# Optimization experiments

Hardware: AMD Instinct MI355X
Metric: run time of the kernel (lower is better)

Reference implementation:

```python
import jax, jax.numpy as jnp
import numpy as np

TAU = 2.0          # LIF membrane time constant
V_THRESHOLD = 1.0  # spikingjelly LIFNode default
V_RESET = 0.0      # hard reset target (spikingjelly default)
ATAN_ALPHA = 2.0   # surrogate.ATan default alpha

T, B, L, D_IN, D_OUT = 16, 32, 128, 512, 512


@jax.custom_vjp
def atan_spike(x):
    # Heaviside forward; ATan surrogate gradient in backward.
    return (x >= 0.0).astype(x.dtype)

def _atan_spike_fwd(x):
    return atan_spike(x), x

def _atan_spike_bwd(x, g):
    # d/dx [ (1/pi) * atan(pi/2 * alpha * x) + 1/2 ]
    grad = (ATAN_ALPHA / 2.0) / (1.0 + (jnp.pi / 2.0 * ATAN_ALPHA * x) ** 2)
    return (g * grad,)

atan_spike.defvjp(_atan_spike_fwd, _atan_spike_bwd)


def lif_multistep(h):
    """Multi-step LIF over leading time axis. h: [T, B, L, H] -> spikes [T, B, L, H].
    spikingjelly LIFNode (decay_input=True, hard reset, detach_reset=True):
      v = v + (x - (v - v_reset)) / tau
      s = heaviside(v - v_threshold)   (ATan surrogate grad)
      v = v_reset * s_detached + v * (1 - s_detached)
    """
    def step(v, x_t):
        v = v + (x_t - (v - V_RESET)) / TAU
        s = atan_spike(v - V_THRESHOLD)
        s_d = jax.lax.stop_gradient(s)  # detach_reset=True
        v = V_RESET * s_d + v * (1.0 - s_d)
        return v, s

    v0 = jnp.zeros_like(h[0])
    _, spikes = jax.lax.scan(step, v0, h)
    return spikes


def setup_inputs() -> dict:
    key = jax.random.key(0)
    kx, kw, kb = jax.random.split(key, 3)
    x = jax.random.normal(kx, (T, B, L, D_IN), dtype=jnp.float32)
    # nn.Linear init: U(-1/sqrt(fan_in), 1/sqrt(fan_in))
    bound = 1.0 / np.sqrt(D_IN)
    W = jax.random.uniform(kw, (D_OUT, D_IN), minval=-bound, maxval=bound, dtype=jnp.float32)
    b = jax.random.uniform(kb, (D_OUT,), minval=-bound, maxval=bound, dtype=jnp.float32)
    return {"x": x, "W": W, "b": b}


def reference(x, W, b):
    # Linear over flattened (T*B) dims == per-element projection, then LIF.
    h = jnp.einsum("tbld,hd->tblh", x, W) + b  # [T, B, L, D_OUT]
    return lif_multistep(h)
```

## Files before the change

### kernel.cpp

```cpp
#include <hip/hip_runtime.h>

using f32x4 = __attribute__((ext_vector_type(4))) float;
using s16x8 = __attribute__((ext_vector_type(8))) short;

constexpr int T_STEPS = 16;
constexpr int BLTOT   = 4096;
constexpr int KDIM    = 512;
constexpr int NDIM    = 512;

constexpr int BM = 128, BN = 128, BK = 32;
constexpr int ROWB  = 80;
constexpr int COMP  = 128 * ROWB;
constexpr int BBASE = 3 * COMP;


__device__ __forceinline__ void split3_write(char* lds, float4 v, int off) {
  unsigned u[4], u1[4], u2[4];
  float r1[4], r2[4];
#pragma unroll
  for (int e = 0; e < 4; ++e) {
    float ve = ((const float*)&v)[e];
    u[e]  = __float_as_uint(ve);
    r1[e] = ve - __uint_as_float(u[e] & 0xFFFF0000u);
    u1[e] = __float_as_uint(r1[e]);
    r2[e] = r1[e] - __uint_as_float(u1[e] & 0xFFFF0000u);
    u2[e] = __float_as_uint(r2[e]);
  }
  uint2 hp, mp, lp;
  hp.x = (u[0]  >> 16) | (u[1]  & 0xFFFF0000u);
  hp.y = (u[2]  >> 16) | (u[3]  & 0xFFFF0000u);
  mp.x = (u1[0] >> 16) | (u1[1] & 0xFFFF0000u);
  mp.y = (u1[2] >> 16) | (u1[3] & 0xFFFF0000u);
  lp.x = (u2[0] >> 16) | (u2[1] & 0xFFFF0000u);
  lp.y = (u2[2] >> 16) | (u2[3] & 0xFFFF0000u);
  *(uint2*)(lds + off)            = hp;
  *(uint2*)(lds + off + COMP)     = mp;
  *(uint2*)(lds + off + 2 * COMP) = lp;
}

__global__ __launch_bounds__(256, 2)
void fused_mfma_lif(const float* __restrict__ x, const float* __restrict__ W,
                    const float* __restrict__ bias, float* __restrict__ out) {
  __shared__ __align__(16) char lds[6 * COMP];

  const int tid  = threadIdx.x;
  const int lane = tid & 63;
  const int wv   = tid >> 6;
  const int wm   = wv >> 1;
  const int wn   = wv & 1;
  const int bl0  = blockIdx.x * 8;
  const int n0   = blockIdx.y * BN;

  const float* aptr[4];
  const float* bptr[4];
  int aw[4], bw[4];
#pragma unroll
  for (int i = 0; i < 4; ++i) {
    int f  = i * 256 + tid;
    int r  = f >> 3;
    int kq = (f & 7) * 4;
    int t  = ((r >> 4) & 3) * 4 + (r & 3);
    int bl = (r >> 6) * 4 + ((r >> 2) & 3);
    aptr[i] = x + (size_t)(t * BLTOT + bl0 + bl) * KDIM + kq;
    bptr[i] = W + (size_t)(n0 + r) * KDIM + kq;
    aw[i] = r * ROWB + kq * 2;
    bw[i] = BBASE + r * ROWB + kq * 2;
  }

  f32x4 acc[4][4];
#pragma unroll
  for (int a = 0; a < 4; ++a)
#pragma unroll
    for (int b = 0; b < 4; ++b) acc[a][b] = (f32x4)(0.0f);

  const int arow = (wm * 64 + (lane & 15)) * ROWB + (lane >> 4) * 16;
  const int brow = BBASE + (wn * 64 + (lane & 15)) * ROWB + (lane >> 4) * 16;

  float4 ar[4], br[4];
#pragma unroll
  for (int i = 0; i < 4; ++i) {
    ar[i] = *(const float4*)(aptr[i]);
    br[i] = *(const float4*)(bptr[i]);
  }

  for (int it = 0; it < 16; ++it) {
    __syncthreads();
#pragma unroll
    for (int i = 0; i < 4; ++i) {
      split3_write(lds, ar[i], aw[i]);
      split3_write(lds, br[i], bw[i]);
    }
    __syncthreads();

    if (it < 15) {
      const int ko = (it + 1) * BK;
#pragma unroll
      for (int i = 0; i < 4; ++i) {
        ar[i] = *(const float4*)(aptr[i] + ko);
        br[i] = *(const float4*)(bptr[i] + ko);
      }
    }

    s16x8 bf[4][3];
#pragma unroll
    for (int nf = 0; nf < 4; ++nf)
#pragma unroll
      for (int c = 0; c < 3; ++c)
        bf[nf][c] = *(const s16x8*)(lds + brow + nf * 16 * ROWB + c * COMP);

#pragma unroll
    for (int mf = 0; mf < 4; ++mf) {
      s16x8 af[3];
#pragma unroll
      for (int c = 0; c < 3; ++c)
        af[c] = *(const s16x8*)(lds + arow + mf * 16 * ROWB + c * COMP);
#pragma unroll
      for (int nf = 0; nf < 4; ++nf) {
        f32x4 c0 = acc[mf][nf];
        c0 = __builtin_amdgcn_mfma_f32_16x16x32_bf16(af[2], bf[nf][0], c0, 0, 0, 0);
        c0 = __builtin_amdgcn_mfma_f32_16x16x32_bf16(af[0], bf[nf][2], c0, 0, 0, 0);
        c0 = __builtin_amdgcn_mfma_f32_16x16x32_bf16(af[1], bf[nf][1], c0, 0, 0, 0);
        c0 = __builtin_amdgcn_mfma_f32_16x16x32_bf16(af[1], bf[nf][0], c0, 0, 0, 0);
        c0 = __builtin_amdgcn_mfma_f32_16x16x32_bf16(af[0], bf[nf][1], c0, 0, 0, 0);
        c0 = __builtin_amdgcn_mfma_f32_16x16x32_bf16(af[0], bf[nf][0], c0, 0, 0, 0);
        acc[mf][nf] = c0;
      }
    }
  }

  const int G   = lane >> 4;
  const int bl  = bl0 + wm * 4 + G;
  const int col = lane & 15;
#pragma unroll
  for (int nf = 0; nf < 4; ++nf) {
    const int n = n0 + wn * 64 + nf * 16 + col;
    const float bb = bias[n];
    float v = 0.0f;
#pragma unroll
    for (int t = 0; t < T_STEPS; ++t) {
      const float h = ((const float*)&acc[t >> 2][nf])[t & 3] + bb;
      float vn = v + (h - v) * 0.5f;
      const bool s = (vn >= 1.0f);
      out[(size_t)(t * BLTOT + bl) * NDIM + n] = s ? 1.0f : 0.0f;
      v = s ? 0.0f : vn;
    }
  }
}

extern "C" void kernel_launch(void* const* d_in, const int* in_sizes, int n_in,
                              void* d_out, int out_size, void* d_ws, size_t ws_size,
                              hipStream_t stream) {
  const float* x = (const float*)d_in[0];
  const float* W = (const float*)d_in[1];
  const float* b = (const float*)d_in[2];
  float* out = (float*)d_out;

  dim3 grid(BLTOT / 8, NDIM / BN);
  fused_mfma_lif<<<grid, 256, 0, stream>>>(x, W, b, out);
}
```

Measured before the change: 448.4 us.

## Pre-split operands into bf16x3 fragment layout in workspace, load directly to LDS

Adds two pre-pass kernels that split x and W into high, mid and low bf16 parts and store them in an MFMA-fragment-ready layout in the workspace. The GEMM+LIF kernel then streams these fragments straight into LDS with global_load_lds, and uses a swizzled block order to improve L2 reuse across the four N-blocks. This removes the repeated per-block split arithmetic and the register-to-LDS scatter from the main loop. In exchange it writes and re-reads a roughly 200 MB workspace, and the main loop is single-buffered with two barriers per iteration. The old fused kernel is kept as a fallback when the workspace is too small.

New measurement: 415.1 us. -7.4%, faster.

```diff
diff --git a/kernel.cpp b/kernel.cpp
--- a/kernel.cpp
+++ b/kernel.cpp
@@ -8,64 +8,91 @@
 constexpr int KDIM    = 512;
 constexpr int NDIM    = 512;
 
-constexpr int BM = 128, BN = 128, BK = 32;
-constexpr int ROWB  = 80;
-constexpr int COMP  = 128 * ROWB;
-constexpr int BBASE = 3 * COMP;
-
-
-__device__ __forceinline__ void split3_write(char* lds, float4 v, int off) {
-  unsigned u[4], u1[4], u2[4];
-  float r1[4], r2[4];
-#pragma unroll
-  for (int e = 0; e < 4; ++e) {
-    float ve = ((const float*)&v)[e];
-    u[e]  = __float_as_uint(ve);
-    r1[e] = ve - __uint_as_float(u[e] & 0xFFFF0000u);
-    u1[e] = __float_as_uint(r1[e]);
-    r2[e] = r1[e] - __uint_as_float(u1[e] & 0xFFFF0000u);
-    u2[e] = __float_as_uint(r2[e]);
-  }
-  uint2 hp, mp, lp;
-  hp.x = (u[0]  >> 16) | (u[1]  & 0xFFFF0000u);
-  hp.y = (u[2]  >> 16) | (u[3]  & 0xFFFF0000u);
-  mp.x = (u1[0] >> 16) | (u1[1] & 0xFFFF0000u);
-  mp.y = (u1[2] >> 16) | (u1[3] & 0xFFFF0000u);
-  lp.x = (u2[0] >> 16) | (u2[1] & 0xFFFF0000u);
-  lp.y = (u2[2] >> 16) | (u2[3] & 0xFFFF0000u);
-  *(uint2*)(lds + off)            = hp;
-  *(uint2*)(lds + off + COMP)     = mp;
-  *(uint2*)(lds + off + 2 * COMP) = lp;
+constexpr size_t B_BYTES = 32ull * 16 * 3 * 1024;
+constexpr size_t A_BYTES = 512ull * 8 * 16 * 3 * 1024;
+constexpr size_t ABASE   = B_BYTES;
+constexpr size_t WS_NEED = A_BYTES + B_BYTES;
+
+
+__device__ __forceinline__ void split8(const float* e, uint4& hp, uint4& mp, uint4& lp) {
+  unsigned h[8], m[8], l[8];
+#pragma unroll
+  for (int j = 0; j < 8; ++j) {
+    const float f = e[j];
+    const unsigned u = __float_as_uint(f);
+    h[j] = u >> 16;
+    const float r1 = f - __uint_as_float(u & 0xFFFF0000u);
+    const unsigned u1 = __float_as_uint(r1);
+    m[j] = u1 >> 16;
+    const float r2 = r1 - __uint_as_float(u1 & 0xFFFF0000u);
+    l[j] = __float_as_uint(r2) >> 16;
+  }
+  hp = make_uint4(h[0] | (h[1] << 16), h[2] | (h[3] << 16),
+                  h[4] | (h[5] << 16), h[6] | (h[7] << 16));
+  mp = make_uint4(m[0] | (m[1] << 16), m[2] | (m[3] << 16),
+                  m[4] | (m[5] << 16), m[6] | (m[7] << 16));
+  lp = make_uint4(l[0] | (l[1] << 16), l[2] | (l[3] << 16),
+                  l[4] | (l[5] << 16), l[6] | (l[7] << 16));
+}
+
+__global__ void split_w(const float* __restrict__ W, char* __restrict__ ws) {
+  const int tid = threadIdx.x;
+  const int wid = blockIdx.x * 4 + (tid >> 6);
+  const int lane = tid & 63;
+  const int nt = wid >> 4, ks = wid & 15;
+  const int q = lane & 15, g = lane >> 4;
+  const float* src = W + (size_t)(nt * 16 + q) * KDIM + ks * 32 + g * 8;
+  float e[8];
+  *(float4*)&e[0] = *(const float4*)src;
+  *(float4*)&e[4] = *(const float4*)(src + 4);
+  uint4 hp, mp, lp;
+  split8(e, hp, mp, lp);
+  char* dst = ws + (size_t)wid * 3072 + lane * 16;
+  *(uint4*)(dst)        = hp;
+  *(uint4*)(dst + 1024) = mp;
+  *(uint4*)(dst + 2048) = lp;
+}
+
+__global__ void split_x(const float* __restrict__ x, char* __restrict__ ws) {
+  const int tid = threadIdx.x;
+  const int wid = blockIdx.x * 4 + (tid >> 6);
+  const int lane = tid & 63;
+  const int ks = wid & 15, mtile = wid >> 4;
+  const int mt = mtile & 7, mb = mtile >> 3;
+  const int q = lane & 15, g = lane >> 4;
+  const int t  = (mt & 3) * 4 + (q & 3);
+  const int bl = mb * 8 + (mt >> 2) * 4 + (q >> 2);
+  const float* src = x + (size_t)(t * BLTOT + bl) * KDIM + ks * 32 + g * 8;
+  float e[8];
+  *(float4*)&e[0] = *(const float4*)src;
+  *(float4*)&e[4] = *(const float4*)(src + 4);
+  uint4 hp, mp, lp;
+  split8(e, hp, mp, lp);
+  char* dst = ws + ABASE + (size_t)wid * 3072 + lane * 16;
+  *(uint4*)(dst)        = hp;
+  *(uint4*)(dst + 1024) = mp;
+  *(uint4*)(dst + 2048) = lp;
 }
 
 __global__ __launch_bounds__(256, 2)
-void fused_mfma_lif(const float* __restrict__ x, const float* __restrict__ W,
-                    const float* __restrict__ bias, float* __restrict__ out) {
-  __shared__ __align__(16) char lds[6 * COMP];
+void gemm_lif_frag(const char* __restrict__ wsB, const char* __restrict__ wsA,
+                   const float* __restrict__ bias, float* __restrict__ out) {
+  __shared__ __align__(16) char lds[48 * 1024];
 
   const int tid  = threadIdx.x;
   const int lane = tid & 63;
   const int wv   = tid >> 6;
-  const int wm   = wv >> 1;
-  const int wn   = wv & 1;
-  const int bl0  = blockIdx.x * 8;
-  const int n0   = blockIdx.y * BN;
-
-  const float* aptr[4];
-  const float* bptr[4];
-  int aw[4], bw[4];
-#pragma unroll
-  for (int i = 0; i < 4; ++i) {
-    int f  = i * 256 + tid;
-    int r  = f >> 3;
-    int kq = (f & 7) * 4;
-    int t  = ((r >> 4) & 3) * 4 + (r & 3);
-    int bl = (r >> 6) * 4 + ((r >> 2) & 3);
-    aptr[i] = x + (size_t)(t * BLTOT + bl0 + bl) * KDIM + kq;
-    bptr[i] = W + (size_t)(n0 + r) * KDIM + kq;
-    aw[i] = r * ROWB + kq * 2;
-    bw[i] = BBASE + r * ROWB + kq * 2;
-  }
+  const int wm   = wv >> 1, wn = wv & 1;
+
+  const int w    = blockIdx.x;
+  const int orig = (w & 7) * 256 + (w >> 3);
+  const int nb   = orig & 3;
+  const int mb   = orig >> 2;
+
+  const bool isA = (wv < 2);
+  const int blk0 = isA ? (mb * 8 + wv * 4) : (nb * 8 + (wv - 2) * 4);
+  const char* gbase = (isA ? wsA : wsB) + (size_t)blk0 * 49152 + lane * 16;
+  char* ldsdst = lds + wv * 12288;
 
   f32x4 acc[4][4];
 #pragma unroll
@@ -73,47 +100,31 @@
 #pragma unroll
     for (int b = 0; b < 4; ++b) acc[a][b] = (f32x4)(0.0f);
 
-  const int arow = (wm * 64 + (lane & 15)) * ROWB + (lane >> 4) * 16;
-  const int brow = BBASE + (wn * 64 + (lane & 15)) * ROWB + (lane >> 4) * 16;
-
-  float4 ar[4], br[4];
-#pragma unroll
-  for (int i = 0; i < 4; ++i) {
-    ar[i] = *(const float4*)(aptr[i]);
-    br[i] = *(const float4*)(bptr[i]);
-  }
-
-  for (int it = 0; it < 16; ++it) {
-    __syncthreads();
-#pragma unroll
-    for (int i = 0; i < 4; ++i) {
-      split3_write(lds, ar[i], aw[i]);
-      split3_write(lds, br[i], bw[i]);
-    }
-    __syncthreads();
-
-    if (it < 15) {
-      const int ko = (it + 1) * BK;
-#pragma unroll
-      for (int i = 0; i < 4; ++i) {
-        ar[i] = *(const float4*)(aptr[i] + ko);
-        br[i] = *(const float4*)(bptr[i] + ko);
-      }
-    }
+  int koff = 0;
+  for (int ksl = 0; ksl < 16; ++ksl) {
+#pragma unroll
+    for (int i = 0; i < 12; ++i) {
+      const int co = ((i / 3) * 48 + (i % 3)) * 1024;
+      __builtin_amdgcn_global_load_lds(
+          (const __attribute__((address_space(1))) void*)(gbase + koff + co),
+          (__attribute__((address_space(3))) void*)(ldsdst + i * 1024), 16, 0, 0);
+    }
+    koff += 3072;
+    __syncthreads();
 
     s16x8 bf[4][3];
 #pragma unroll
     for (int nf = 0; nf < 4; ++nf)
 #pragma unroll
       for (int c = 0; c < 3; ++c)
-        bf[nf][c] = *(const s16x8*)(lds + brow + nf * 16 * ROWB + c * COMP);
+        bf[nf][c] = *(const s16x8*)(lds + 24576 + ((wn * 4 + nf) * 3 + c) * 1024 + lane * 16);
 
 #pragma unroll
     for (int mf = 0; mf < 4; ++mf) {
       s16x8 af[3];
 #pragma unroll
       for (int c = 0; c < 3; ++c)
-        af[c] = *(const s16x8*)(lds + arow + mf * 16 * ROWB + c * COMP);
+        af[c] = *(const s16x8*)(lds + ((wm * 4 + mf) * 3 + c) * 1024 + lane * 16);
 #pragma unroll
       for (int nf = 0; nf < 4; ++nf) {
         f32x4 c0 = acc[mf][nf];
@@ -126,11 +137,13 @@
         acc[mf][nf] = c0;
       }
     }
+    __syncthreads();
   }
 
   const int G   = lane >> 4;
-  const int bl  = bl0 + wm * 4 + G;
+  const int bl  = mb * 8 + wm * 4 + G;
   const int col = lane & 15;
+  const int n0  = nb * 128;
 #pragma unroll
   for (int nf = 0; nf < 4; ++nf) {
     const int n = n0 + wn * 64 + nf * 16 + col;
@@ -139,7 +152,121 @@
 #pragma unroll
     for (int t = 0; t < T_STEPS; ++t) {
       const float h = ((const float*)&acc[t >> 2][nf])[t & 3] + bb;
-      float vn = v + (h - v) * 0.5f;
+      const float vn = v + (h - v) * 0.5f;
+      const bool s = (vn >= 1.0f);
+      out[(size_t)(t * BLTOT + bl) * NDIM + n] = s ? 1.0f : 0.0f;
+      v = s ? 0.0f : vn;
+    }
+  }
+}
+
+constexpr int FB_ROWB  = 80;
+constexpr int FB_COMP  = 128 * FB_ROWB;
+constexpr int FB_BBASE = 3 * FB_COMP;
+
+__device__ __forceinline__ void split3_write(char* lds, float4 v, int off) {
+  unsigned u[4], u1[4], u2[4];
+#pragma unroll
+  for (int e = 0; e < 4; ++e) {
+    float ve = ((const float*)&v)[e];
+    u[e]  = __float_as_uint(ve);
+    float r1 = ve - __uint_as_float(u[e] & 0xFFFF0000u);
+    u1[e] = __float_as_uint(r1);
+    float r2 = r1 - __uint_as_float(u1[e] & 0xFFFF0000u);
+    u2[e] = __float_as_uint(r2);
+  }
+  uint2 hp, mp, lp;
+  hp.x = (u[0]  >> 16) | (u[1]  & 0xFFFF0000u);
+  hp.y = (u[2]  >> 16) | (u[3]  & 0xFFFF0000u);
+  mp.x = (u1[0] >> 16) | (u1[1] & 0xFFFF0000u);
+  mp.y = (u1[2] >> 16) | (u1[3] & 0xFFFF0000u);
+  lp.x = (u2[0] >> 16) | (u2[1] & 0xFFFF0000u);
+  lp.y = (u2[2] >> 16) | (u2[3] & 0xFFFF0000u);
+  *(uint2*)(lds + off)               = hp;
+  *(uint2*)(lds + off + FB_COMP)     = mp;
+  *(uint2*)(lds + off + 2 * FB_COMP) = lp;
+}
+
+__global__ __launch_bounds__(256, 2)
+void fused_mfma_lif_fb(const float* __restrict__ x, const float* __restrict__ W,
+                       const float* __restrict__ bias, float* __restrict__ out) {
+  __shared__ __align__(16) char lds[6 * FB_COMP];
+  const int tid = threadIdx.x;
+  const int lane = tid & 63;
+  const int wv = tid >> 6, wm = wv >> 1, wn = wv & 1;
+  const int bl0 = blockIdx.x * 8, n0 = blockIdx.y * 128;
+
+  const float* aptr[4]; const float* bptr[4];
+  int aw[4], bw[4];
+#pragma unroll
+  for (int i = 0; i < 4; ++i) {
+    int f = i * 256 + tid, r = f >> 3, kq = (f & 7) * 4;
+    int t = ((r >> 4) & 3) * 4 + (r & 3);
+    int bl = (r >> 6) * 4 + ((r >> 2) & 3);
+    aptr[i] = x + (size_t)(t * BLTOT + bl0 + bl) * KDIM + kq;
+    bptr[i] = W + (size_t)(n0 + r) * KDIM + kq;
+    aw[i] = r * FB_ROWB + kq * 2;
+    bw[i] = FB_BBASE + r * FB_ROWB + kq * 2;
+  }
+  f32x4 acc[4][4];
+#pragma unroll
+  for (int a = 0; a < 4; ++a)
+#pragma unroll
+    for (int b = 0; b < 4; ++b) acc[a][b] = (f32x4)(0.0f);
+
+  const int arow = (wm * 64 + (lane & 15)) * FB_ROWB + (lane >> 4) * 16;
+  const int brow = FB_BBASE + (wn * 64 + (lane & 15)) * FB_ROWB + (lane >> 4) * 16;
+
+  float4 ar[4], br[4];
+#pragma unroll
+  for (int i = 0; i < 4; ++i) { ar[i] = *(const float4*)(aptr[i]); br[i] = *(const float4*)(bptr[i]); }
+
+  for (int it = 0; it < 16; ++it) {
+    __syncthreads();
+#pragma unroll
+    for (int i = 0; i < 4; ++i) { split3_write(lds, ar[i], aw[i]); split3_write(lds, br[i], bw[i]); }
+    __syncthreads();
+    if (it < 15) {
+      const int ko = (it + 1) * 32;
+#pragma unroll
+      for (int i = 0; i < 4; ++i) { ar[i] = *(const float4*)(aptr[i] + ko); br[i] = *(const float4*)(bptr[i] + ko); }
+    }
+    s16x8 bf[4][3];
+#pragma unroll
+    for (int nf = 0; nf < 4; ++nf)
+#pragma unroll
+      for (int c = 0; c < 3; ++c)
+        bf[nf][c] = *(const s16x8*)(lds + brow + nf * 16 * FB_ROWB + c * FB_COMP);
+#pragma unroll
+    for (int mf = 0; mf < 4; ++mf) {
+      s16x8 af[3];
+#pragma unroll
+      for (int c = 0; c < 3; ++c)
+        af[c] = *(const s16x8*)(lds + arow + mf * 16 * FB_ROWB + c * FB_COMP);
+#pragma unroll
+      for (int nf = 0; nf < 4; ++nf) {
+        f32x4 c0 = acc[mf][nf];
+        c0 = __builtin_amdgcn_mfma_f32_16x16x32_bf16(af[2], bf[nf][0], c0, 0, 0, 0);
+        c0 = __builtin_amdgcn_mfma_f32_16x16x32_bf16(af[0], bf[nf][2], c0, 0, 0, 0);
+        c0 = __builtin_amdgcn_mfma_f32_16x16x32_bf16(af[1], bf[nf][1], c0, 0, 0, 0);
+        c0 = __builtin_amdgcn_mfma_f32_16x16x32_bf16(af[1], bf[nf][0], c0, 0, 0, 0);
+        c0 = __builtin_amdgcn_mfma_f32_16x16x32_bf16(af[0], bf[nf][1], c0, 0, 0, 0);
+        c0 = __builtin_amdgcn_mfma_f32_16x16x32_bf16(af[0], bf[nf][0], c0, 0, 0, 0);
+        acc[mf][nf] = c0;
+      }
+    }
+  }
+  const int G = lane >> 4, col = lane & 15;
+  const int bl = bl0 + wm * 4 + G;
+#pragma unroll
+  for (int nf = 0; nf < 4; ++nf) {
+    const int n = n0 + wn * 64 + nf * 16 + col;
+    const float bb = bias[n];
+    float v = 0.0f;
+#pragma unroll
+    for (int t = 0; t < T_STEPS; ++t) {
+      const float h = ((const float*)&acc[t >> 2][nf])[t & 3] + bb;
+      const float vn = v + (h - v) * 0.5f;
       const bool s = (vn >= 1.0f);
       out[(size_t)(t * BLTOT + bl) * NDIM + n] = s ? 1.0f : 0.0f;
       v = s ? 0.0f : vn;
@@ -155,6 +282,13 @@
   const float* b = (const float*)d_in[2];
   float* out = (float*)d_out;
 
-  dim3 grid(BLTOT / 8, NDIM / BN);
-  fused_mfma_lif<<<grid, 256, 0, stream>>>(x, W, b, out);
-}
+  if (ws_size >= WS_NEED) {
+    char* ws = (char*)d_ws;
+    split_w<<<128, 256, 0, stream>>>(W, ws);
+    split_x<<<16384, 256, 0, stream>>>(x, ws);
+    gemm_lif_frag<<<2048, 256, 0, stream>>>(ws, ws + ABASE, b, out);
+  } else {
+    dim3 grid(BLTOT / 8, NDIM / 128);
+    fused_mfma_lif_fb<<<grid, 256, 0, stream>>>(x, W, b, out);
+  }
+}
```
